# Performance work log

Measured on AMD Instinct MI355X. Metric: run time of the kernel, lower is better.

Reference implementation:

```python
import jax, jax.numpy as jnp
import numpy as np

B, C, H, W = 4, 96, 64, 64
CS = 8                      # chunk size
DN = 2 * C                  # d_inner (expand=2)
N = 16                      # d_state
K = 4                       # scan directions
DT_R = (C + 15) // 16       # dt_rank = ceil(d_model/16)
EPS = 1e-5


def _ln(x, g, b):
    m = x.mean(-1, keepdims=True)
    v = ((x - m) ** 2).mean(-1, keepdims=True)
    return (x - m) / jnp.sqrt(v + EPS) * g + b


def _selective_scan(xs, delta, A, Bs, Cs, D):
    # xs, delta: (Bc, K, Dn, L); Bs, Cs: (Bc, K, N, L); A: (K, Dn, N); D: (K, Dn)
    Bc, Kk, Dn, L = xs.shape
    uT = xs.transpose(3, 0, 1, 2)       # (L, Bc, K, Dn)
    dT = delta.transpose(3, 0, 1, 2)
    BT = Bs.transpose(3, 0, 1, 2)       # (L, Bc, K, N)
    CT = Cs.transpose(3, 0, 1, 2)

    def step(h, inp):
        u_l, d_l, B_l, C_l = inp
        dA = jnp.exp(d_l[..., None] * A)                       # (Bc,K,Dn,N)
        h = h * dA + (d_l * u_l)[..., None] * B_l[:, :, None, :]
        y = jnp.einsum('bkdn,bkn->bkd', h, C_l)
        return h, y

    h0 = jnp.zeros((Bc, Kk, Dn, A.shape[-1]), xs.dtype)
    _, ys = jax.lax.scan(step, h0, (uT, dT, BT, CT))           # ys: (L,Bc,K,Dn)
    ys = ys.transpose(1, 2, 3, 0)                              # (Bc,K,Dn,L)
    return ys + D[None, :, :, None] * xs


def _ss2d(xh, in_proj_w, conv_w, conv_b, x_proj_w, dt_w, dt_b,
          A_logs, Ds, outnorm_g, outnorm_b, out_proj_w):
    # xh: (Bc, Hc, Wc, C)
    Bc, Hc, Wc, _ = xh.shape
    L = Hc * Wc
    xz = xh @ in_proj_w                                        # (Bc,Hc,Wc,2*Dn)
    xc, z = jnp.split(xz, 2, axis=-1)
    xc = xc.transpose(0, 3, 1, 2)                              # (Bc,Dn,Hc,Wc)
    xc = jax.lax.conv_general_dilated(xc, conv_w, (1, 1), ((1, 1), (1, 1)),
                                      feature_group_count=DN)
    xc = jax.nn.silu(xc + conv_b[None, :, None, None])
    x0 = xc.reshape(Bc, DN, L)                                 # HW order
    x1 = xc.transpose(0, 1, 3, 2).reshape(Bc, DN, L)           # WH order
    xs = jnp.stack([x0, x1, x0[:, :, ::-1], x1[:, :, ::-1]], axis=1)  # (Bc,4,Dn,L)
    x_dbl = jnp.einsum('bkdl,kcd->bkcl', xs, x_proj_w)         # (Bc,4,DT_R+2N,L)
    dts = x_dbl[:, :, :DT_R]
    Bs = x_dbl[:, :, DT_R:DT_R + N]
    Cs = x_dbl[:, :, DT_R + N:]
    dts = jnp.einsum('bkrl,kdr->bkdl', dts, dt_w)
    delta = jax.nn.softplus(dts + dt_b[None, :, :, None])      # (Bc,4,Dn,L)
    A = -jnp.exp(A_logs).reshape(K, DN, N)
    ys = _selective_scan(xs, delta, A, Bs, Cs, Ds.reshape(K, DN))
    y0 = ys[:, 0]
    y1 = ys[:, 1].reshape(Bc, DN, Wc, Hc).transpose(0, 1, 3, 2).reshape(Bc, DN, L)
    y2 = ys[:, 2, :, ::-1]
    y3 = ys[:, 3, :, ::-1].reshape(Bc, DN, Wc, Hc).transpose(0, 1, 3, 2).reshape(Bc, DN, L)
    y = (y0 + y1 + y2 + y3).transpose(0, 2, 1)                 # (Bc,L,Dn)
    y = _ln(y, outnorm_g, outnorm_b).reshape(Bc, Hc, Wc, DN)
    y = y * jax.nn.silu(z)
    return y @ out_proj_w                                      # (Bc,Hc,Wc,C)


def reference(x, gamma, beta, alpha, ln1_g, ln1_b, in_proj_w, conv_w, conv_b,
              x_proj_w, dt_w, dt_b, A_logs, Ds, outnorm_g, outnorm_b, out_proj_w):
    Bb, Cc, Hh, Ww = x.shape
    # StateNorm: per (b, c) over spatial dims, unbiased=False
    mean = x.mean(axis=(2, 3), keepdims=True)
    var = ((x - mean) ** 2).mean(axis=(2, 3), keepdims=True)
    x_norm = (x - mean) / jnp.sqrt(var + EPS)
    x_norm = gamma[None, :, None, None] * x_norm + beta[None, :, None, None]
    x_act = jax.nn.silu(x_norm)                 # act_quant with bits=32 is identity
    hn, wn = Hh // CS, Ww // CS
    # chunk: b c (hn cs)(wn cs) -> (b hn wn) c cs cs
    xc = x_act.reshape(Bb, Cc, hn, CS, wn, CS).transpose(0, 2, 4, 1, 3, 5)
    xc = xc.reshape(Bb * hn * wn, Cc, CS, CS)
    # VSSBlock: h + SS2D(LN(h)) in BHWC (drop_path = identity at inference)
    h = xc.transpose(0, 2, 3, 1)                # (Bc, cs, cs, C)
    h = h + _ss2d(_ln(h, ln1_g, ln1_b), in_proj_w, conv_w, conv_b, x_proj_w,
                  dt_w, dt_b, A_logs, Ds, outnorm_g, outnorm_b, out_proj_w)
    xv = h.transpose(0, 3, 1, 2)                # back to BCHW
    # unchunk
    xv = xv.reshape(Bb, hn, wn, Cc, CS, CS).transpose(0, 3, 1, 4, 2, 5)
    xv = xv.reshape(Bb, Cc, Hh, Ww)
    return x + alpha * xv


def setup_inputs() -> dict:
    key = jax.random.key(0)
    ks = jax.random.split(key, 12)
    s = 0.02
    inp = {
        'x': jax.random.normal(ks[0], (B, C, H, W), jnp.float32),
        'gamma': jnp.ones((C,), jnp.float32),
        'beta': jnp.zeros((C,), jnp.float32),
        'alpha': jnp.float32(0.5),
        'ln1_g': jnp.ones((C,), jnp.float32),
        'ln1_b': jnp.zeros((C,), jnp.float32),
        'in_proj_w': jax.random.normal(ks[1], (C, 2 * DN), jnp.float32) / np.sqrt(C),
        'conv_w': jax.random.normal(ks[2], (DN, 1, 3, 3), jnp.float32) / 3.0,
        'conv_b': jnp.zeros((DN,), jnp.float32),
        'x_proj_w': jax.random.normal(ks[3], (K, DT_R + 2 * N, DN), jnp.float32) / np.sqrt(DN),
        'dt_w': jax.random.normal(ks[4], (K, DN, DT_R), jnp.float32) * (DT_R ** -0.5),
        'dt_b': jnp.full((K, DN), -4.6, jnp.float32) + s * jax.random.normal(ks[5], (K, DN), jnp.float32),
        'A_logs': jnp.log(jnp.broadcast_to(jnp.arange(1, N + 1, dtype=jnp.float32), (K * DN, N))).copy(),
        'Ds': jnp.ones((K * DN,), jnp.float32),
        'outnorm_g': jnp.ones((DN,), jnp.float32),
        'outnorm_b': jnp.zeros((DN,), jnp.float32),
        'out_proj_w': jax.random.normal(ks[6], (DN, C), jnp.float32) / np.sqrt(DN),
    }
    return inp
```

## Files before the change

kernel.cpp:

```cpp
#include <hip/hip_runtime.h>
#include <math.h>

#define NCHUNK 256
#define PROW   40

__device__ __forceinline__ float siluf_(float x) {
    return x / (1.f + __expf(-x));
}

__device__ __forceinline__ int sperm(int k, int l) {
    int t = (k & 1) ? (((l & 7) << 3) | (l >> 3)) : l;
    return (k & 2) ? (63 - t) : t;
}

__global__ void k1a_stats(const float* __restrict__ x, float* __restrict__ stats) {
    int bc = blockIdx.x;
    const float* xp = x + (size_t)bc * 4096;
    float s = 0.f, sq = 0.f;
    for (int i = threadIdx.x; i < 4096; i += 256) {
        float v = xp[i]; s += v; sq += v * v;
    }
    __shared__ float rs[256], rq[256];
    rs[threadIdx.x] = s; rq[threadIdx.x] = sq;
    __syncthreads();
    for (int off = 128; off > 0; off >>= 1) {
        if (threadIdx.x < off) {
            rs[threadIdx.x] += rs[threadIdx.x + off];
            rq[threadIdx.x] += rq[threadIdx.x + off];
        }
        __syncthreads();
    }
    if (threadIdx.x == 0) {
        float m = rs[0] * (1.f / 4096.f);
        float v = rq[0] * (1.f / 4096.f) - m * m;
        stats[bc] = m;
        stats[384 + bc] = rsqrtf(v + 1e-5f);
    }
}

__global__ __launch_bounds__(256) void kA(
        const float* __restrict__ x, const float* __restrict__ stats,
        const float* __restrict__ gamma, const float* __restrict__ beta,
        const float* __restrict__ ln1_g, const float* __restrict__ ln1_b,
        const float* __restrict__ Win,
        float* __restrict__ xcg_all,
        float* __restrict__ zg_all) {
    int blk = blockIdx.x;
    int chunk = blk >> 2, cg = blk & 3;
    int b = chunk >> 6, chh = (chunk >> 3) & 7, chw = chunk & 7;
    __shared__ float hs[64 * 97];
    int t = threadIdx.x;
    for (int i = t; i < 6144; i += 256) {
        int c = i >> 6, pos = i & 63;
        int bc = b * 96 + c;
        int hh = chh * 8 + (pos >> 3), ww = chw * 8 + (pos & 7);
        float v = x[(((size_t)bc) * 64 + hh) * 64 + ww];
        float xn = (v - stats[bc]) * stats[384 + bc] * gamma[c] + beta[c];
        hs[pos * 97 + c] = siluf_(xn);
    }
    __syncthreads();
    {
        int p = t >> 2, o = t & 3;
        float s = 0.f, sq = 0.f;
        #pragma unroll
        for (int j = 0; j < 24; j++) { float v = hs[p * 97 + o + 4 * j]; s += v; sq += v * v; }
        s += __shfl_xor(s, 1); sq += __shfl_xor(sq, 1);
        s += __shfl_xor(s, 2); sq += __shfl_xor(sq, 2);
        float m = s * (1.f / 96.f);
        float rinv = rsqrtf(sq * (1.f / 96.f) - m * m + 1e-5f);
        #pragma unroll
        for (int j = 0; j < 24; j++) {
            int c = o + 4 * j;
            hs[p * 97 + c] = (hs[p * 97 + c] - m) * rinv * ln1_g[c] + ln1_b[c];
        }
    }
    __syncthreads();
    int p = t & 63;
    int wv = __builtin_amdgcn_readfirstlane(t >> 6);
    int jbase = cg * 96 + wv * 24;
    float acc[24];
    #pragma unroll
    for (int i = 0; i < 24; i++) acc[i] = 0.f;
    for (int c = 0; c < 96; c++) {
        float u = hs[p * 97 + c];
        const float* w = Win + c * 384 + jbase;
        #pragma unroll
        for (int i = 0; i < 24; i++) acc[i] = fmaf(u, w[i], acc[i]);
    }
    if (jbase < 192) {
        float* o_ = xcg_all + (size_t)chunk * 12288 + jbase * 64 + p;
        #pragma unroll
        for (int i = 0; i < 24; i++) o_[i * 64] = acc[i];
    } else {
        float* o_ = zg_all + (size_t)chunk * 12288 + (jbase - 192) * 64 + p;
        #pragma unroll
        for (int i = 0; i < 24; i++) o_[i * 64] = acc[i];
    }
}

__global__ __launch_bounds__(256) void kB(
        const float* __restrict__ xcg_all, const float* __restrict__ conv_w,
        const float* __restrict__ conv_b, float* __restrict__ x0T_all) {
    int blk = blockIdx.x;
    int chunk = blk >> 2, dg = blk & 3;
    int dbase = dg * 48;
    __shared__ float tile[48 * 65];
    int t = threadIdx.x;
    const float* in = xcg_all + (size_t)chunk * 12288 + dbase * 64;
    for (int i = t; i < 3072; i += 256) tile[(i >> 6) * 65 + (i & 63)] = in[i];
    __syncthreads();
    float* o = x0T_all + (size_t)chunk * 12288;
    for (int s = 0; s < 12; s++) {
        int idx = s * 256 + t;
        int l = idx / 48, dl = idx - l * 48;
        int r = l >> 3, cc = l & 7;
        int d = dbase + dl;
        float acc = conv_b[d];
        #pragma unroll
        for (int dh = 0; dh < 3; dh++) {
            int rr = r + dh - 1;
            if (rr < 0 || rr > 7) continue;
            #pragma unroll
            for (int dw = 0; dw < 3; dw++) {
                int cw = cc + dw - 1;
                if (cw < 0 || cw > 7) continue;
                acc = fmaf(tile[dl * 65 + rr * 8 + cw], conv_w[d * 9 + dh * 3 + dw], acc);
            }
        }
        o[l * 192 + d] = siluf_(acc);
    }
}

__global__ __launch_bounds__(192) void kD(
        const float* __restrict__ x0T_all, const float* __restrict__ xpw,
        const float* __restrict__ dtw, const float* __restrict__ dtb,
        const float* __restrict__ A_logs, const float* __restrict__ Ds,
        float* __restrict__ Pg_all,
        float* __restrict__ yac_all) {
    int blk = blockIdx.x;
    int chunk = blk >> 2, k = blk & 3;
    __shared__ float pT[64 * 41];
    int t = threadIdx.x;
    const float* xbase = x0T_all + (size_t)chunk * 12288;

    {
        int l = t & 63;
        int wv = __builtin_amdgcn_readfirstlane(t >> 6);
        int cbase = wv * 13;
        float acc[13];
        #pragma unroll
        for (int i = 0; i < 13; i++) acc[i] = 0.f;
        const float* xl = xbase + l * 192;
        const float* wb = xpw + (size_t)k * 38 * 192;
        for (int dd = 0; dd < 192; dd += 4) {
            float4 u4 = *(const float4*)(xl + dd);
            #pragma unroll
            for (int ci = 0; ci < 13; ci++) {
                int c = cbase + ci;
                if (c < 38) {
                    float4 w4 = *(const float4*)(wb + c * 192 + dd);
                    acc[ci] = fmaf(u4.x, w4.x, acc[ci]);
                    acc[ci] = fmaf(u4.y, w4.y, acc[ci]);
                    acc[ci] = fmaf(u4.z, w4.z, acc[ci]);
                    acc[ci] = fmaf(u4.w, w4.w, acc[ci]);
                }
            }
        }
        #pragma unroll
        for (int ci = 0; ci < 13; ci++) {
            int c = cbase + ci;
            if (c < 38) {
                int slot = c + (c >= 6 ? 2 : 0);
                pT[l * 41 + slot] = acc[ci];
            }
        }
    }
    __syncthreads();
    float* pgout = Pg_all + (size_t)blk * 2560;
    for (int i = t; i < 2560; i += 192) {
        int l = i / 40, s = i - l * 40;
        pgout[i] = pT[l * 41 + s];
    }
    __syncthreads();

    {
        int d = t;
        int gd = k * 192 + d;
        float w6[6];
        #pragma unroll
        for (int r = 0; r < 6; r++) w6[r] = dtw[gd * 6 + r];
        float bias = dtb[gd];
        float Dd = Ds[gd];
        float a[16];
        #pragma unroll
        for (int n = 0; n < 16; n++) a[n] = -__expf(A_logs[gd * 16 + n]);
        bool pw = true;
        #pragma unroll
        for (int n = 1; n < 16; n++)
            pw = pw && (fabsf(a[n] - (float)(n + 1) * a[0]) <= 1e-4f * fabsf(a[n]) + 1e-6f);
        float hst[16];
        #pragma unroll
        for (int n = 0; n < 16; n++) hst[n] = 0.f;
        const float* pbase = pgout;
        float* yo = yac_all + (size_t)chunk * 12288;

        if (__all(pw)) {
            float a0 = a[0];
            float u_nxt = xbase[sperm(k, 0) * 192 + d];
            for (int l = 0; l < 64; l++) {
                int sl = sperm(k, l);
                float u = u_nxt;
                if (l < 63) u_nxt = xbase[sperm(k, l + 1) * 192 + d];
                const float* row = pbase + sl * PROW;
                float dp = bias;
                #pragma unroll
                for (int r = 0; r < 6; r++) dp = fmaf(row[r], w6[r], dp);
                float delta = (dp > 20.f) ? dp : __logf(1.f + __expf(dp));
                float du = delta * u;
                float e1 = __expf(delta * a0);
                float p[16];
                p[0] = e1;
                p[1] = e1 * e1;
                p[2] = p[1] * e1;   p[3] = p[1] * p[1];
                p[4] = p[3] * e1;   p[5] = p[3] * p[1];
                p[6] = p[3] * p[2]; p[7] = p[3] * p[3];
                p[8] = p[7] * e1;   p[9] = p[7] * p[1];
                p[10] = p[7] * p[2]; p[11] = p[7] * p[3];
                p[12] = p[7] * p[4]; p[13] = p[7] * p[5];
                p[14] = p[7] * p[6]; p[15] = p[7] * p[7];
                float y0 = 0.f, y1 = 0.f, y2 = 0.f, y3 = 0.f;
                #pragma unroll
                for (int n = 0; n < 16; n += 4) {
                    hst[n]     = fmaf(hst[n],     p[n],     du * row[8 + n]);
                    hst[n + 1] = fmaf(hst[n + 1], p[n + 1], du * row[9 + n]);
                    hst[n + 2] = fmaf(hst[n + 2], p[n + 2], du * row[10 + n]);
                    hst[n + 3] = fmaf(hst[n + 3], p[n + 3], du * row[11 + n]);
                    y0 = fmaf(hst[n],     row[24 + n], y0);
                    y1 = fmaf(hst[n + 1], row[25 + n], y1);
                    y2 = fmaf(hst[n + 2], row[26 + n], y2);
                    y3 = fmaf(hst[n + 3], row[27 + n], y3);
                }
                atomicAdd(&yo[sl * 192 + d], (y0 + y1) + (y2 + y3) + Dd * u);
            }
        } else {
            for (int l = 0; l < 64; l++) {
                int sl = sperm(k, l);
                float u = xbase[sl * 192 + d];
                const float* row = pbase + sl * PROW;
                float dp = bias;
                #pragma unroll
                for (int r = 0; r < 6; r++) dp = fmaf(row[r], w6[r], dp);
                float delta = (dp > 20.f) ? dp : __logf(1.f + __expf(dp));
                float du = delta * u;
                float y = 0.f;
                #pragma unroll
                for (int n = 0; n < 16; n++) {
                    float e = __expf(delta * a[n]);
                    hst[n] = fmaf(hst[n], e, du * row[8 + n]);
                    y = fmaf(hst[n], row[24 + n], y);
                }
                atomicAdd(&yo[sl * 192 + d], y + Dd * u);
            }
        }
    }
}

__global__ __launch_bounds__(256) void kE(
        const float* __restrict__ yac_all, const float* __restrict__ zg_all,
        const float* __restrict__ og, const float* __restrict__ ob,
        float* __restrict__ g_all) {
    int blk = blockIdx.x;
    int chunk = blk >> 1, half = blk & 1;
    int t = threadIdx.x;
    int p = half * 32 + (t >> 3), o = t & 7;
    const float* yrow = yac_all + (size_t)chunk * 12288 + p * 192;
    float ys[24];
    float s = 0.f, sq = 0.f;
    #pragma unroll
    for (int j = 0; j < 24; j++) {
        float v = yrow[o + 8 * j];
        ys[j] = v; s += v; sq += v * v;
    }
    s += __shfl_xor(s, 1); sq += __shfl_xor(sq, 1);
    s += __shfl_xor(s, 2); sq += __shfl_xor(sq, 2);
    s += __shfl_xor(s, 4); sq += __shfl_xor(sq, 4);
    float m = s * (1.f / 192.f);
    float rinv = rsqrtf(sq * (1.f / 192.f) - m * m + 1e-5f);
    const float* z = zg_all + (size_t)chunk * 12288;
    float* g = g_all + (size_t)chunk * 12288;
    #pragma unroll
    for (int j = 0; j < 24; j++) {
        int i = o + 8 * j;
        float ln = (ys[j] - m) * rinv * og[i] + ob[i];
        g[i * 64 + p] = ln * siluf_(z[i * 64 + p]);
    }
}

__global__ __launch_bounds__(256) void kF(
        const float* __restrict__ g_all, const float* __restrict__ Wout,
        const float* __restrict__ x, const float* __restrict__ stats,
        const float* __restrict__ gamma, const float* __restrict__ beta,
        const float* __restrict__ alpha, float* __restrict__ out) {
    int blk = blockIdx.x;
    int chunk = blk >> 2, cgf = blk & 3;
    int b = chunk >> 6, chh = (chunk >> 3) & 7, chw = chunk & 7;
    int t = threadIdx.x;
    int p = t & 63;
    int wv = __builtin_amdgcn_readfirstlane(t >> 6);
    int cbase = cgf * 24 + wv * 6;
    float acc[6];
    #pragma unroll
    for (int i = 0; i < 6; i++) acc[i] = 0.f;
    const float* g = g_all + (size_t)chunk * 12288;
    for (int dd = 0; dd < 192; dd++) {
        float u = g[dd * 64 + p];
        const float* w = Wout + dd * 96 + cbase;
        #pragma unroll
        for (int i = 0; i < 6; i++) acc[i] = fmaf(u, w[i], acc[i]);
    }
    float al = alpha[0];
    int hh = chh * 8 + (p >> 3), ww = chw * 8 + (p & 7);
    #pragma unroll
    for (int i = 0; i < 6; i++) {
        int c = cbase + i;
        int bc = b * 96 + c;
        size_t gi = (((size_t)bc) * 64 + hh) * 64 + ww;
        float xv = x[gi];
        float xn = (xv - stats[bc]) * stats[384 + bc] * gamma[c] + beta[c];
        out[gi] = xv + al * (siluf_(xn) + acc[i]);
    }
}

extern "C" void kernel_launch(void* const* d_in, const int* in_sizes, int n_in,
                              void* d_out, int out_size, void* d_ws, size_t ws_size,
                              hipStream_t stream) {
    const float* x        = (const float*)d_in[0];
    const float* gamma    = (const float*)d_in[1];
    const float* beta     = (const float*)d_in[2];
    const float* alpha    = (const float*)d_in[3];
    const float* ln1_g    = (const float*)d_in[4];
    const float* ln1_b    = (const float*)d_in[5];
    const float* in_proj  = (const float*)d_in[6];
    const float* conv_w   = (const float*)d_in[7];
    const float* conv_b   = (const float*)d_in[8];
    const float* x_proj   = (const float*)d_in[9];
    const float* dt_w     = (const float*)d_in[10];
    const float* dt_b     = (const float*)d_in[11];
    const float* A_logs   = (const float*)d_in[12];
    const float* Ds       = (const float*)d_in[13];
    const float* onorm_g  = (const float*)d_in[14];
    const float* onorm_b  = (const float*)d_in[15];
    const float* out_proj = (const float*)d_in[16];
    float* out = (float*)d_out;

    float* ws    = (float*)d_ws;
    float* stats = ws;
    float* xcg   = ws + 768;
    float* zg    = xcg + 3145728;
    float* x0T   = zg + 3145728;
    float* Pg    = x0T + 3145728;
    float* yac   = xcg;
    float* gbuf  = x0T;

    hipLaunchKernelGGL(k1a_stats, dim3(384), dim3(256), 0, stream, x, stats);
    hipLaunchKernelGGL(kA, dim3(1024), dim3(256), 0, stream,
                       x, stats, gamma, beta, ln1_g, ln1_b, in_proj, xcg, zg);
    hipLaunchKernelGGL(kB, dim3(1024), dim3(256), 0, stream,
                       xcg, conv_w, conv_b, x0T);
    hipMemsetAsync(yac, 0, (size_t)3145728 * 4, stream);
    hipLaunchKernelGGL(kD, dim3(1024), dim3(192), 0, stream,
                       x0T, x_proj, dt_w, dt_b, A_logs, Ds, Pg, yac);
    hipLaunchKernelGGL(kE, dim3(512), dim3(256), 0, stream,
                       yac, zg, onorm_g, onorm_b, gbuf);
    hipLaunchKernelGGL(kF, dim3(1024), dim3(256), 0, stream,
                       gbuf, out_proj, x, stats, gamma, beta, alpha, out);
}
```

Measured before the change: 227.0 us.

## Accumulate scan outputs in LDS per direction pair, store z and partials as bf16

The scan kernel now handles two directions per block, with 384 threads. It accumulates y into shared memory instead of global atomics, folds the D*x skip term into the initial accumulator, and drops the memset. One direction pair writes fp32 partials and the other writes packed bf16, and the gate z is also stored as bf16 to halve its traffic. Block indices are remapped so consecutive chunks land on the same XCD for L2 locality. The bf16 storage loses precision in z and in half of the y sum, and the larger shared footprint may reduce occupancy.

```diff
diff --git a/kernel.cpp b/kernel.cpp
--- a/kernel.cpp
+++ b/kernel.cpp
@@ -1,8 +1,7 @@
 #include <hip/hip_runtime.h>
 #include <math.h>
 
-#define NCHUNK 256
-#define PROW   40
+#define PROW 40
 
 __device__ __forceinline__ float siluf_(float x) {
     return x / (1.f + __expf(-x));
@@ -11,6 +10,17 @@
 __device__ __forceinline__ int sperm(int k, int l) {
     int t = (k & 1) ? (((l & 7) << 3) | (l >> 3)) : l;
     return (k & 2) ? (63 - t) : t;
+}
+
+__device__ __forceinline__ unsigned int f2bf(float f) {
+    unsigned int u = __float_as_uint(f);
+    return (u + 0x7FFFu + ((u >> 16) & 1u)) >> 16;
+}
+__device__ __forceinline__ float bf2f(unsigned int h) {
+    return __uint_as_float(h << 16);
+}
+__device__ __forceinline__ unsigned int packbf(float lo, float hi) {
+    return f2bf(lo) | (f2bf(hi) << 16);
 }
 
 __global__ void k1a_stats(const float* __restrict__ x, float* __restrict__ stats) {
@@ -44,9 +54,10 @@
         const float* __restrict__ ln1_g, const float* __restrict__ ln1_b,
         const float* __restrict__ Win,
         float* __restrict__ xcg_all,
-        float* __restrict__ zg_all) {
+        unsigned int* __restrict__ zg_b) {
     int blk = blockIdx.x;
-    int chunk = blk >> 2, cg = blk & 3;
+    int xcd = blk & 7, j = blk >> 3;
+    int chunk = xcd * 32 + (j >> 2), cg = j & 3;
     int b = chunk >> 6, chh = (chunk >> 3) & 7, chw = chunk & 7;
     __shared__ float hs[64 * 97];
     int t = threadIdx.x;
@@ -63,14 +74,14 @@
         int p = t >> 2, o = t & 3;
         float s = 0.f, sq = 0.f;
         #pragma unroll
-        for (int j = 0; j < 24; j++) { float v = hs[p * 97 + o + 4 * j]; s += v; sq += v * v; }
+        for (int jj = 0; jj < 24; jj++) { float v = hs[p * 97 + o + 4 * jj]; s += v; sq += v * v; }
         s += __shfl_xor(s, 1); sq += __shfl_xor(sq, 1);
         s += __shfl_xor(s, 2); sq += __shfl_xor(sq, 2);
         float m = s * (1.f / 96.f);
         float rinv = rsqrtf(sq * (1.f / 96.f) - m * m + 1e-5f);
         #pragma unroll
-        for (int j = 0; j < 24; j++) {
-            int c = o + 4 * j;
+        for (int jj = 0; jj < 24; jj++) {
+            int c = o + 4 * jj;
             hs[p * 97 + c] = (hs[p * 97 + c] - m) * rinv * ln1_g[c] + ln1_b[c];
         }
     }
@@ -92,9 +103,10 @@
         #pragma unroll
         for (int i = 0; i < 24; i++) o_[i * 64] = acc[i];
     } else {
-        float* o_ = zg_all + (size_t)chunk * 12288 + (jbase - 192) * 64 + p;
-        #pragma unroll
-        for (int i = 0; i < 24; i++) o_[i * 64] = acc[i];
+        int i2base = (jbase - 192) >> 1;
+        unsigned int* o_ = zg_b + (size_t)chunk * 6144 + i2base * 64 + p;
+        #pragma unroll
+        for (int i = 0; i < 12; i++) o_[i * 64] = packbf(acc[2 * i], acc[2 * i + 1]);
     }
 }
 
@@ -102,7 +114,8 @@
         const float* __restrict__ xcg_all, const float* __restrict__ conv_w,
         const float* __restrict__ conv_b, float* __restrict__ x0T_all) {
     int blk = blockIdx.x;
-    int chunk = blk >> 2, dg = blk & 3;
+    int xcd = blk & 7, j = blk >> 3;
+    int chunk = xcd * 32 + (j >> 2), dg = j & 3;
     int dbase = dg * 48;
     __shared__ float tile[48 * 65];
     int t = threadIdx.x;
@@ -131,22 +144,35 @@
     }
 }
 
-__global__ __launch_bounds__(192) void kD(
+__global__ __launch_bounds__(384, 3) void kD(
         const float* __restrict__ x0T_all, const float* __restrict__ xpw,
         const float* __restrict__ dtw, const float* __restrict__ dtb,
         const float* __restrict__ A_logs, const float* __restrict__ Ds,
         float* __restrict__ Pg_all,
-        float* __restrict__ yac_all) {
+        float* __restrict__ yp0_all,
+        unsigned int* __restrict__ yp1_b) {
     int blk = blockIdx.x;
-    int chunk = blk >> 2, k = blk & 3;
-    __shared__ float pT[64 * 41];
+    int xcd = blk & 7, j = blk >> 3;
+    int chunk = xcd * 32 + (j >> 1);
+    int pair = j & 1;
+    __shared__ float yac[64 * 192];
+    __shared__ float pT[2][64 * 41];
     int t = threadIdx.x;
     const float* xbase = x0T_all + (size_t)chunk * 12288;
+    int g = __builtin_amdgcn_readfirstlane(t / 192);
+    int tk = t - g * 192;
+    int k = pair * 2 + g;
+
+    for (int i = t; i < 12288; i += 384) {
+        int d = i % 192;
+        float dsum = Ds[pair * 384 + d] + Ds[pair * 384 + 192 + d];
+        yac[i] = dsum * xbase[i];
+    }
 
     {
-        int l = t & 63;
-        int wv = __builtin_amdgcn_readfirstlane(t >> 6);
-        int cbase = wv * 13;
+        int l = tk & 63;
+        int wv3 = __builtin_amdgcn_readfirstlane(tk >> 6);
+        int cbase = wv3 * 13;
         float acc[13];
         #pragma unroll
         for (int i = 0; i < 13; i++) acc[i] = 0.f;
@@ -171,26 +197,23 @@
             int c = cbase + ci;
             if (c < 38) {
                 int slot = c + (c >= 6 ? 2 : 0);
-                pT[l * 41 + slot] = acc[ci];
+                pT[g][l * 41 + slot] = acc[ci];
             }
         }
     }
     __syncthreads();
-    float* pgout = Pg_all + (size_t)blk * 2560;
-    for (int i = t; i < 2560; i += 192) {
-        int l = i / 40, s = i - l * 40;
-        pgout[i] = pT[l * 41 + s];
-    }
+    float* pgout = Pg_all + (size_t)(chunk * 4 + k) * 2560;
+    for (int i = tk; i < 2560; i += 192)
+        pgout[i] = pT[g][(i / 40) * 41 + (i % 40)];
     __syncthreads();
 
     {
-        int d = t;
+        int d = tk;
         int gd = k * 192 + d;
         float w6[6];
         #pragma unroll
         for (int r = 0; r < 6; r++) w6[r] = dtw[gd * 6 + r];
         float bias = dtb[gd];
-        float Dd = Ds[gd];
         float a[16];
         #pragma unroll
         for (int n = 0; n < 16; n++) a[n] = -__expf(A_logs[gd * 16 + n]);
@@ -201,8 +224,7 @@
         float hst[16];
         #pragma unroll
         for (int n = 0; n < 16; n++) hst[n] = 0.f;
-        const float* pbase = pgout;
-        float* yo = yac_all + (size_t)chunk * 12288;
+        const float* pbase = Pg_all + (size_t)(chunk * 4 + k) * 2560;
 
         if (__all(pw)) {
             float a0 = a[0];
@@ -240,7 +262,7 @@
                     y2 = fmaf(hst[n + 2], row[26 + n], y2);
                     y3 = fmaf(hst[n + 3], row[27 + n], y3);
                 }
-                atomicAdd(&yo[sl * 192 + d], (y0 + y1) + (y2 + y3) + Dd * u);
+                atomicAdd(&yac[sl * 192 + d], (y0 + y1) + (y2 + y3));
             }
         } else {
             for (int l = 0; l < 64; l++) {
@@ -259,40 +281,58 @@
                     hst[n] = fmaf(hst[n], e, du * row[8 + n]);
                     y = fmaf(hst[n], row[24 + n], y);
                 }
-                atomicAdd(&yo[sl * 192 + d], y + Dd * u);
+                atomicAdd(&yac[sl * 192 + d], y);
             }
         }
     }
+    __syncthreads();
+
+    if (pair == 0) {
+        float* yo = yp0_all + (size_t)chunk * 12288;
+        for (int i = t; i < 12288; i += 384) yo[i] = yac[i];
+    } else {
+        unsigned int* yo = yp1_b + (size_t)chunk * 6144;
+        for (int i = t; i < 6144; i += 384)
+            yo[i] = packbf(yac[2 * i], yac[2 * i + 1]);
+    }
 }
 
 __global__ __launch_bounds__(256) void kE(
-        const float* __restrict__ yac_all, const float* __restrict__ zg_all,
+        const float* __restrict__ yp0_all, const unsigned int* __restrict__ yp1_b,
+        const unsigned int* __restrict__ zg_b,
         const float* __restrict__ og, const float* __restrict__ ob,
         float* __restrict__ g_all) {
     int blk = blockIdx.x;
-    int chunk = blk >> 1, half = blk & 1;
+    int xcd = blk & 7, j = blk >> 3;
+    int chunk = xcd * 32 + (j >> 1), half = j & 1;
     int t = threadIdx.x;
     int p = half * 32 + (t >> 3), o = t & 7;
-    const float* yrow = yac_all + (size_t)chunk * 12288 + p * 192;
+    int par = o & 1;
+    const float* yrow = yp0_all + (size_t)chunk * 12288 + p * 192;
+    const unsigned int* y1row = yp1_b + (size_t)chunk * 6144 + p * 96;
     float ys[24];
     float s = 0.f, sq = 0.f;
     #pragma unroll
-    for (int j = 0; j < 24; j++) {
-        float v = yrow[o + 8 * j];
-        ys[j] = v; s += v; sq += v * v;
+    for (int jj = 0; jj < 24; jj++) {
+        int i = o + 8 * jj;
+        unsigned int w = y1row[i >> 1];
+        float v = yrow[i] + bf2f(par ? (w >> 16) : (w & 0xFFFFu));
+        ys[jj] = v; s += v; sq += v * v;
     }
     s += __shfl_xor(s, 1); sq += __shfl_xor(sq, 1);
     s += __shfl_xor(s, 2); sq += __shfl_xor(sq, 2);
     s += __shfl_xor(s, 4); sq += __shfl_xor(sq, 4);
     float m = s * (1.f / 192.f);
     float rinv = rsqrtf(sq * (1.f / 192.f) - m * m + 1e-5f);
-    const float* z = zg_all + (size_t)chunk * 12288;
+    const unsigned int* z = zg_b + (size_t)chunk * 6144;
     float* g = g_all + (size_t)chunk * 12288;
     #pragma unroll
-    for (int j = 0; j < 24; j++) {
-        int i = o + 8 * j;
-        float ln = (ys[j] - m) * rinv * og[i] + ob[i];
-        g[i * 64 + p] = ln * siluf_(z[i * 64 + p]);
+    for (int jj = 0; jj < 24; jj++) {
+        int i = o + 8 * jj;
+        float ln = (ys[jj] - m) * rinv * og[i] + ob[i];
+        unsigned int zw = z[(i >> 1) * 64 + p];
+        float zv = bf2f(par ? (zw >> 16) : (zw & 0xFFFFu));
+        g[i * 64 + p] = ln * siluf_(zv);
     }
 }
 
@@ -302,7 +342,8 @@
         const float* __restrict__ gamma, const float* __restrict__ beta,
         const float* __restrict__ alpha, float* __restrict__ out) {
     int blk = blockIdx.x;
-    int chunk = blk >> 2, cgf = blk & 3;
+    int xcd = blk & 7, j = blk >> 3;
+    int chunk = xcd * 32 + (j >> 2), cgf = j & 3;
     int b = chunk >> 6, chh = (chunk >> 3) & 7, chw = chunk & 7;
     int t = threadIdx.x;
     int p = t & 63;
@@ -356,22 +397,22 @@
     float* ws    = (float*)d_ws;
     float* stats = ws;
     float* xcg   = ws + 768;
-    float* zg    = xcg + 3145728;
-    float* x0T   = zg + 3145728;
+    float* x0T   = xcg + 3145728;
     float* Pg    = x0T + 3145728;
-    float* yac   = xcg;
+    unsigned int* zg_b  = (unsigned int*)(Pg + 2621440);
+    unsigned int* yp1_b = zg_b + 1572864;
+    float* yp0   = xcg;
     float* gbuf  = x0T;
 
     hipLaunchKernelGGL(k1a_stats, dim3(384), dim3(256), 0, stream, x, stats);
     hipLaunchKernelGGL(kA, dim3(1024), dim3(256), 0, stream,
-                       x, stats, gamma, beta, ln1_g, ln1_b, in_proj, xcg, zg);
+                       x, stats, gamma, beta, ln1_g, ln1_b, in_proj, xcg, zg_b);
     hipLaunchKernelGGL(kB, dim3(1024), dim3(256), 0, stream,
                        xcg, conv_w, conv_b, x0T);
-    hipMemsetAsync(yac, 0, (size_t)3145728 * 4, stream);
-    hipLaunchKernelGGL(kD, dim3(1024), dim3(192), 0, stream,
-                       x0T, x_proj, dt_w, dt_b, A_logs, Ds, Pg, yac);
+    hipLaunchKernelGGL(kD, dim3(512), dim3(384), 0, stream,
+                       x0T, x_proj, dt_w, dt_b, A_logs, Ds, Pg, yp0, yp1_b);
     hipLaunchKernelGGL(kE, dim3(512), dim3(256), 0, stream,
-                       yac, zg, onorm_g, onorm_b, gbuf);
+                       yp0, yp1_b, zg_b, onorm_g, onorm_b, gbuf);
     hipLaunchKernelGGL(kF, dim3(1024), dim3(256), 0, stream,
                        gbuf, out_proj, x, stats, gamma, beta, alpha, out);
 }
```

After: 266.5 us. 1.17x slower.
